# Kernel optimization log

Hardware: AMD Instinct MI355X
Metric: run time of the kernel (lower is better)

## Reference

```python
import jax, jax.numpy as jnp
import numpy as np

B = 8192   # batch of independent theta draws (ABM calibration ensemble)
T = 4096   # recurrence length (__init__ T)
THETA_DIM = 11  # beta, g1..g4, b1..b4, sigma, r


def setup_inputs() -> dict:
    key = jax.random.key(0)
    k1, k2 = jax.random.split(key)
    # uniform[0,1) guarantees beta>0, sigma>0, r>=0 as asserted in the module
    theta = jax.random.uniform(k1, (B, THETA_DIM), dtype=jnp.float32)
    epsilons = jax.random.normal(k2, (B, T), dtype=jnp.float32)
    return {"theta": theta, "epsilons": epsilons}


def reference(theta, epsilons):
    # Brock-Hommes recurrence (Eqs. 39-40 of arXiv:2202.00625), vmapped over batch.
    beta = theta[:, 0]        # [B]
    g = theta[:, 1:5]         # [B,4]
    b = theta[:, 5:9]         # [B,4]
    sigma = theta[:, 9]       # [B]
    r = theta[:, 10]          # [B]
    R = 1.0 + r               # [B]

    def step(carry, eps_t):
        x1, x2, x3 = carry    # x[t-1], x[t-2], x[t-3], each [B]
        Rx2 = R * x2
        # exponent: [B,4]
        exponent = (beta * (x1 - Rx2))[:, None] * (g * x3[:, None] + b - Rx2[:, None])
        w = jax.nn.softmax(exponent, axis=-1)                 # [B,4]
        mean = jnp.sum(w * (g * x1[:, None] + b), axis=-1)    # [B]
        x_t = (mean + eps_t * sigma) / R                      # [B]
        return (x_t, x1, x2), x_t

    z = jnp.zeros(theta.shape[0], dtype=theta.dtype)
    # initial carry of zeros matches x[-1]=x[-2]=x[-3]=0 in the torch code
    _, xs = jax.lax.scan(step, (z, z, z), epsilons.T)  # xs: [T,B]
    return xs.T  # [B,T]
```

## Files before the change

### kernel.cpp

```cpp
#include <hip/hip_runtime.h>

#define THETA_DIM 11
#define BQ   16
#define TILE 64
#define EPAD 68

__device__ __forceinline__ float qdpp_b1(float v) {
  return __builtin_bit_cast(float,
      __builtin_amdgcn_update_dpp(0, __builtin_bit_cast(int, v), 0xB1, 0xF, 0xF, true));
}
__device__ __forceinline__ float qdpp_4e(float v) {
  return __builtin_bit_cast(float,
      __builtin_amdgcn_update_dpp(0, __builtin_bit_cast(int, v), 0x4E, 0xF, 0xF, true));
}
__device__ __forceinline__ float quad_max(float v) {
  v = fmaxf(v, qdpp_b1(v));
  v = fmaxf(v, qdpp_4e(v));
  return v;
}
__device__ __forceinline__ float quad_sum(float v) {
  v = v + qdpp_b1(v);
  v = v + qdpp_4e(v);
  return v;
}
__device__ __forceinline__ float exp2_fast(float x) {
  float r;
  asm("v_exp_f32 %0, %1" : "=v"(r) : "v"(x));
  return r;
}

__device__ __forceinline__ float bh_step(
    float e, float& x1, float& x2, float& x3,
    float& Rx2, float& blRx2, float& q,
    float bl2e, float bl2eR, float R, float g, float bb,
    float gR, float bR, float sR) {
  const float A   = fmaf(bl2e, x1, -blRx2);
  const float tj  = A * q;
  const float m   = quad_max(tj);
  const float p   = exp2_fast(tj - m);
  const float cc  = fmaf(gR, x1, bR);
  const float num = quad_sum(p * cc);
  const float den = quad_sum(p);
  const float invden = __builtin_amdgcn_rcpf(den);
  const float es  = e * sR;
  const float x   = fmaf(num, invden, es);
  x3 = x2; x2 = x1; x1 = x;
  Rx2   = R * x2;
  blRx2 = bl2eR * x2;
  q     = fmaf(g, x3, bb) - Rx2;
  return x;
}

__global__ void __launch_bounds__(64, 1)
bh_kernel(const float* __restrict__ theta, const float* __restrict__ eps,
          float* __restrict__ out, int Tn) {
  __shared__ float eps_s[2][BQ][EPAD];
  __shared__ float out_s[BQ][EPAD];

  const int lane = threadIdx.x;
  const int c  = lane >> 2;
  const int j  = lane & 3;
  const int cb = blockIdx.x * BQ;
  const int b  = cb + c;

  const float* th = theta + b * THETA_DIM;
  const float beta = th[0];
  const float g    = th[1 + j];
  const float bb   = th[5 + j];
  const float sig  = th[9];
  const float r    = th[10];
  const float R    = 1.0f + r;
  const float invR = 1.0f / R;
  const float L2E  = 1.4426950408889634f;
  const float bl2e = beta * L2E;
  const float bl2eR = bl2e * R;
  const float gR = g * invR;
  const float bR = bb * invR;
  const float sR = sig * invR;

  const int col  = lane & 15;
  const int rsub = lane >> 4;

  const int NT = Tn / TILE;

  #pragma unroll
  for (int i = 0; i < 4; ++i) {
    const float4 v = *(const float4*)(eps + (size_t)(cb + i*4 + rsub) * Tn + col*4);
    *(float4*)&eps_s[0][i*4 + rsub][col*4] = v;
  }

  float x1 = 0.f, x2 = 0.f, x3 = 0.f;
  float Rx2 = 0.f, blRx2 = 0.f, q = bb;

  const bool j0 = (j == 0), j1 = (j == 1), j2 = (j == 2);

  for (int tile = 0; tile < NT; ++tile) {
    const int buf = tile & 1;
    const int t0  = tile * TILE;
    const bool more = (tile + 1 < NT);

    float4 pre[4];
    if (more) {
      #pragma unroll
      for (int i = 0; i < 4; ++i)
        pre[i] = *(const float4*)(eps + (size_t)(cb + i*4 + rsub) * Tn
                                  + (t0 + TILE) + col*4);
    }

    const float* ec = &eps_s[buf][c][0];
    float* oc = &out_s[c][0];

    #pragma unroll 4
    for (int t4 = 0; t4 < TILE/4; ++t4) {
      const float4 e4 = *(const float4*)(ec + t4*4);
      const float xw0 = bh_step(e4.x, x1,x2,x3, Rx2,blRx2,q, bl2e,bl2eR,R,g,bb,gR,bR,sR);
      const float xw1 = bh_step(e4.y, x1,x2,x3, Rx2,blRx2,q, bl2e,bl2eR,R,g,bb,gR,bR,sR);
      const float xw2 = bh_step(e4.z, x1,x2,x3, Rx2,blRx2,q, bl2e,bl2eR,R,g,bb,gR,bR,sR);
      const float xw3 = bh_step(e4.w, x1,x2,x3, Rx2,blRx2,q, bl2e,bl2eR,R,g,bb,gR,bR,sR);
      const float xw = j0 ? xw0 : (j1 ? xw1 : (j2 ? xw2 : xw3));
      oc[t4*4 + j] = xw;
    }

    #pragma unroll
    for (int i = 0; i < 4; ++i) {
      const float4 o4 = *(const float4*)&out_s[i*4 + rsub][col*4];
      *(float4*)(out + (size_t)(cb + i*4 + rsub) * Tn + t0 + col*4) = o4;
    }

    if (more) {
      #pragma unroll
      for (int i = 0; i < 4; ++i)
        *(float4*)&eps_s[buf ^ 1][i*4 + rsub][col*4] = pre[i];
    }
  }
}

extern "C" void kernel_launch(void* const* d_in, const int* in_sizes, int n_in,
                              void* d_out, int out_size, void* d_ws, size_t ws_size,
                              hipStream_t stream) {
  const float* theta = (const float*)d_in[0];
  const float* eps   = (const float*)d_in[1];
  float* out = (float*)d_out;
  const int B  = in_sizes[0] / THETA_DIM;
  const int Tn = in_sizes[1] / B;
  const int blocks = B / BQ;
  bh_kernel<<<blocks, 64, 0, stream>>>(theta, eps, out, Tn);
}
```

Measured before the change: 514.8 us.

## Precompute softmax max via sign-split q extrema, load eps directly per lane

Replaces the per-step quad max over the exponent with a sign-based choice between precomputed (q - max q) and (q - min q), which are computed one step ahead off the critical dependency chain. This is valid because the exponent is A*q with A shared across the quad. Epsilon is now loaded straight from global memory into registers two float4 groups ahead, replacing the LDS double buffer. The aim is to shorten the serial latency chain of each recurrence step, at the cost of redundant global loads across the four lanes of each quad.

```diff
diff --git a/kernel.cpp b/kernel.cpp
--- a/kernel.cpp
+++ b/kernel.cpp
@@ -3,7 +3,7 @@
 #define THETA_DIM 11
 #define BQ   16
 #define TILE 64
-#define EPAD 68
+#define OPAD 68
 
 __device__ __forceinline__ float qdpp_b1(float v) {
   return __builtin_bit_cast(float,
@@ -14,48 +14,44 @@
       __builtin_amdgcn_update_dpp(0, __builtin_bit_cast(int, v), 0x4E, 0xF, 0xF, true));
 }
 __device__ __forceinline__ float quad_max(float v) {
-  v = fmaxf(v, qdpp_b1(v));
-  v = fmaxf(v, qdpp_4e(v));
-  return v;
+  v = fmaxf(v, qdpp_b1(v)); v = fmaxf(v, qdpp_4e(v)); return v;
+}
+__device__ __forceinline__ float quad_min(float v) {
+  v = fminf(v, qdpp_b1(v)); v = fminf(v, qdpp_4e(v)); return v;
 }
 __device__ __forceinline__ float quad_sum(float v) {
-  v = v + qdpp_b1(v);
-  v = v + qdpp_4e(v);
-  return v;
-}
-__device__ __forceinline__ float exp2_fast(float x) {
-  float r;
-  asm("v_exp_f32 %0, %1" : "=v"(r) : "v"(x));
-  return r;
+  v = v + qdpp_b1(v); v = v + qdpp_4e(v); return v;
 }
 
 __device__ __forceinline__ float bh_step(
-    float e, float& x1, float& x2, float& x3,
-    float& Rx2, float& blRx2, float& q,
-    float bl2e, float bl2eR, float R, float g, float bb,
-    float gR, float bR, float sR) {
-  const float A   = fmaf(bl2e, x1, -blRx2);
-  const float tj  = A * q;
-  const float m   = quad_max(tj);
-  const float p   = exp2_fast(tj - m);
-  const float cc  = fmaf(gR, x1, bR);
-  const float num = quad_sum(p * cc);
+    float es, float& x1, float& x2,
+    float& c1, float& dqM, float& dqm, float& cc,
+    float bl2e, float bl2eR, float negR, float g, float bb,
+    float gR, float bR) {
+  const float A  = fmaf(bl2e, x1, -c1);
+  const float dq = (A >= 0.0f) ? dqM : dqm;
+  const float t  = A * dq;
+  const float p  = __builtin_amdgcn_exp2f(t);
+  const float pc = p * cc;
+  const float num = quad_sum(pc);
   const float den = quad_sum(p);
-  const float invden = __builtin_amdgcn_rcpf(den);
-  const float es  = e * sR;
-  const float x   = fmaf(num, invden, es);
-  x3 = x2; x2 = x1; x1 = x;
-  Rx2   = R * x2;
-  blRx2 = bl2eR * x2;
-  q     = fmaf(g, x3, bb) - Rx2;
+  const float x  = fmaf(num, __builtin_amdgcn_rcpf(den), es);
+  const float qn  = fmaf(negR, x1, fmaf(g, x2, bb));
+  const float c1n = bl2eR * x1;
+  const float qmaxn = quad_max(qn);
+  const float qminn = quad_min(qn);
+  dqM = qn - qmaxn;
+  dqm = qn - qminn;
+  c1  = c1n;
+  x2  = x1; x1 = x;
+  cc  = fmaf(gR, x, bR);
   return x;
 }
 
 __global__ void __launch_bounds__(64, 1)
 bh_kernel(const float* __restrict__ theta, const float* __restrict__ eps,
           float* __restrict__ out, int Tn) {
-  __shared__ float eps_s[2][BQ][EPAD];
-  __shared__ float out_s[BQ][EPAD];
+  __shared__ float out_s[BQ][OPAD];
 
   const int lane = threadIdx.x;
   const int c  = lane >> 2;
@@ -72,65 +68,59 @@
   const float R    = 1.0f + r;
   const float invR = 1.0f / R;
   const float L2E  = 1.4426950408889634f;
-  const float bl2e = beta * L2E;
+  const float bl2e  = beta * L2E;
   const float bl2eR = bl2e * R;
+  const float negR  = -R;
   const float gR = g * invR;
   const float bR = bb * invR;
   const float sR = sig * invR;
 
+  float x1 = 0.f, x2 = 0.f;
+  float c1 = 0.f;
+  float q0 = bb;
+  float qmax0 = quad_max(q0), qmin0 = quad_min(q0);
+  float dqM = q0 - qmax0, dqm = q0 - qmin0;
+  float cc = bR;
+
+  const float* ep = eps + (size_t)b * Tn;
+  const int tlast = Tn - 4;
+  float4 eA = *(const float4*)(ep + 0);
+  float4 eB = *(const float4*)(ep + 4);
+
   const int col  = lane & 15;
   const int rsub = lane >> 4;
 
-  const int NT = Tn / TILE;
-
-  #pragma unroll
-  for (int i = 0; i < 4; ++i) {
-    const float4 v = *(const float4*)(eps + (size_t)(cb + i*4 + rsub) * Tn + col*4);
-    *(float4*)&eps_s[0][i*4 + rsub][col*4] = v;
-  }
-
-  float x1 = 0.f, x2 = 0.f, x3 = 0.f;
-  float Rx2 = 0.f, blRx2 = 0.f, q = bb;
-
   const bool j0 = (j == 0), j1 = (j == 1), j2 = (j == 2);
 
+  int t = 0;
+  const int NT = Tn / TILE;
   for (int tile = 0; tile < NT; ++tile) {
-    const int buf = tile & 1;
-    const int t0  = tile * TILE;
-    const bool more = (tile + 1 < NT);
-
-    float4 pre[4];
-    if (more) {
-      #pragma unroll
-      for (int i = 0; i < 4; ++i)
-        pre[i] = *(const float4*)(eps + (size_t)(cb + i*4 + rsub) * Tn
-                                  + (t0 + TILE) + col*4);
-    }
-
-    const float* ec = &eps_s[buf][c][0];
     float* oc = &out_s[c][0];
 
     #pragma unroll 4
-    for (int t4 = 0; t4 < TILE/4; ++t4) {
-      const float4 e4 = *(const float4*)(ec + t4*4);
-      const float xw0 = bh_step(e4.x, x1,x2,x3, Rx2,blRx2,q, bl2e,bl2eR,R,g,bb,gR,bR,sR);
-      const float xw1 = bh_step(e4.y, x1,x2,x3, Rx2,blRx2,q, bl2e,bl2eR,R,g,bb,gR,bR,sR);
-      const float xw2 = bh_step(e4.z, x1,x2,x3, Rx2,blRx2,q, bl2e,bl2eR,R,g,bb,gR,bR,sR);
-      const float xw3 = bh_step(e4.w, x1,x2,x3, Rx2,blRx2,q, bl2e,bl2eR,R,g,bb,gR,bR,sR);
+    for (int g4 = 0; g4 < TILE / 4; ++g4) {
+      const float4 ecur = eA;
+      eA = eB;
+      int tn = t + 8; tn = (tn > tlast) ? tlast : tn;
+      eB = *(const float4*)(ep + tn);
+      const float es0 = ecur.x * sR, es1 = ecur.y * sR;
+      const float es2 = ecur.z * sR, es3 = ecur.w * sR;
+
+      const float xw0 = bh_step(es0, x1,x2, c1,dqM,dqm,cc, bl2e,bl2eR,negR,g,bb,gR,bR);
+      const float xw1 = bh_step(es1, x1,x2, c1,dqM,dqm,cc, bl2e,bl2eR,negR,g,bb,gR,bR);
+      const float xw2 = bh_step(es2, x1,x2, c1,dqM,dqm,cc, bl2e,bl2eR,negR,g,bb,gR,bR);
+      const float xw3 = bh_step(es3, x1,x2, c1,dqM,dqm,cc, bl2e,bl2eR,negR,g,bb,gR,bR);
+
       const float xw = j0 ? xw0 : (j1 ? xw1 : (j2 ? xw2 : xw3));
-      oc[t4*4 + j] = xw;
+      oc[g4 * 4 + j] = xw;
+      t += 4;
     }
 
+    const int t0 = tile * TILE;
     #pragma unroll
     for (int i = 0; i < 4; ++i) {
       const float4 o4 = *(const float4*)&out_s[i*4 + rsub][col*4];
       *(float4*)(out + (size_t)(cb + i*4 + rsub) * Tn + t0 + col*4) = o4;
-    }
-
-    if (more) {
-      #pragma unroll
-      for (int i = 0; i < 4; ++i)
-        *(float4*)&eps_s[buf ^ 1][i*4 + rsub][col*4] = pre[i];
     }
   }
 }
```

Result: slower. 542.0 us (+5.3%).
